# Optimization experiments

Hardware: AMD Instinct MI355X
Metric: run time of the kernel (lower is better)

## Reference

```python
import jax, jax.numpy as jnp
import numpy as np


def setup_inputs() -> dict:
    key = jax.random.key(0)
    k1, k2 = jax.random.split(key)
    B, F, L = 2048, 1, 512       # batch, n_features, seq_len
    N = 100000                   # fitted training windows
    x_enc = jax.random.normal(k1, (B, F, L), dtype=jnp.float32)
    X_fit = jax.random.normal(k2, (N, F * L), dtype=jnp.float32)
    return {"x_enc": x_enc, "X_fit": X_fit, "n_neighbors": 5}


def reference(x_enc, X_fit, n_neighbors):
    # x_enc: [B, F, L]; X_fit: [N, F*L]
    B, F, L = x_enc.shape
    q = x_enc.reshape(B, -1)                       # [B, D]
    # Squared Euclidean distances: ||q||^2 + ||x||^2 - 2 q.x^T  -> [B, N]
    q_sq = jnp.sum(q * q, axis=-1, keepdims=True)           # [B, 1]
    x_sq = jnp.sum(X_fit * X_fit, axis=-1)[None, :]         # [1, N]
    d2 = q_sq + x_sq - 2.0 * jnp.einsum("bd,nd->bn", q, X_fit)
    # k nearest = k smallest distances
    _, idx = jax.lax.top_k(-d2, n_neighbors)                # idx: [B, k]
    neigh = X_fit[idx]                                      # [B, k, D]
    y_hat = jnp.mean(neigh, axis=1).reshape(B, F, L)        # neighbor mean
    return y_hat
```

## Files before the change

kernel.cpp:

```cpp
#include <hip/hip_runtime.h>
#include <float.h>

#define D 512
#define BM 128
#define BN 256
#define BK 32
#define NCH 64
#define MPC 8
#define TR 16

typedef __attribute__((ext_vector_type(8))) short short8;
typedef __attribute__((ext_vector_type(4))) float f32x4;
typedef const __attribute__((address_space(1))) void gv_t;
typedef __attribute__((address_space(3))) void lv_t;

__device__ __forceinline__ void gl2lds16(const void* g, void* l) {
    __builtin_amdgcn_global_load_lds((gv_t*)g, (lv_t*)l, 16, 0, 0);
}

__device__ __forceinline__ unsigned short f2bf(float f) {
    unsigned u = __float_as_uint(f);
    return (unsigned short)((u + 0x7FFF + ((u >> 16) & 1)) >> 16);
}

template <int K>
__device__ __forceinline__ void insertK(float* bs, int* bi, float v, int id) {
    if (v < bs[K - 1]) {
        bs[K - 1] = v; bi[K - 1] = id;
#pragma unroll
        for (int r = K - 1; r >= 1; --r) {
            if (bs[r] < bs[r - 1]) {
                float tf = bs[r]; bs[r] = bs[r - 1]; bs[r - 1] = tf;
                int ti = bi[r]; bi[r] = bi[r - 1]; bi[r - 1] = ti;
            }
        }
    }
}

__global__ void convert_x(const float* __restrict__ X, unsigned short* __restrict__ Xbf,
                          float* __restrict__ xsq, int N, int padN) {
    int row = blockIdx.x * 4 + (threadIdx.x >> 6);
    int lane = threadIdx.x & 63;
    if (row >= padN) return;
    unsigned short ob[8];
    float s = 0.0f;
    if (row < N) {
        const float* p = X + (size_t)row * D + lane * 8;
        float4 a = *(const float4*)p;
        float4 b = *(const float4*)(p + 4);
        s = a.x * a.x + a.y * a.y + a.z * a.z + a.w * a.w
          + b.x * b.x + b.y * b.y + b.z * b.z + b.w * b.w;
        ob[0] = f2bf(a.x); ob[1] = f2bf(a.y); ob[2] = f2bf(a.z); ob[3] = f2bf(a.w);
        ob[4] = f2bf(b.x); ob[5] = f2bf(b.y); ob[6] = f2bf(b.z); ob[7] = f2bf(b.w);
    } else {
#pragma unroll
        for (int i = 0; i < 8; ++i) ob[i] = 0;
    }
    *(uint4*)(Xbf + (size_t)row * D + lane * 8) = *(uint4*)ob;
#pragma unroll
    for (int off = 32; off > 0; off >>= 1) s += __shfl_down(s, off, 64);
    if (lane == 0) xsq[row] = (row < N) ? s : 1e30f;
}

__global__ void convert_q(const float* __restrict__ Q, unsigned short* __restrict__ Qbf) {
    int row = blockIdx.x * 4 + (threadIdx.x >> 6);
    int lane = threadIdx.x & 63;
    const float* p = Q + (size_t)row * D + lane * 8;
    float4 a = *(const float4*)p;
    float4 b = *(const float4*)(p + 4);
    unsigned short ob[8];
    ob[0] = f2bf(-2.0f * a.x); ob[1] = f2bf(-2.0f * a.y);
    ob[2] = f2bf(-2.0f * a.z); ob[3] = f2bf(-2.0f * a.w);
    ob[4] = f2bf(-2.0f * b.x); ob[5] = f2bf(-2.0f * b.y);
    ob[6] = f2bf(-2.0f * b.z); ob[7] = f2bf(-2.0f * b.w);
    *(uint4*)(Qbf + (size_t)row * D + lane * 8) = *(uint4*)ob;
}

struct KBuf { unsigned short A[BM * BK]; unsigned short B[BN * BK]; };

#define STAGE(bp_, nn0, kk0)                                                          \
    do {                                                                              \
        const size_t kof_ = (size_t)(kk0) + sseg;                                     \
        gl2lds16(Qbf + (size_t)(qrow0 + srow) * D + kof_, (bp_)->A + wave * 512);     \
        gl2lds16(Qbf + (size_t)(qrow0 + 64 + srow) * D + kof_,                        \
                 (bp_)->A + 2048 + wave * 512);                                       \
        gl2lds16(Xbf + (size_t)((nn0) + srow) * D + kof_, (bp_)->B + wave * 512);     \
        gl2lds16(Xbf + (size_t)((nn0) + 64 + srow) * D + kof_,                        \
                 (bp_)->B + 2048 + wave * 512);                                       \
        gl2lds16(Xbf + (size_t)((nn0) + 128 + srow) * D + kof_,                       \
                 (bp_)->B + 4096 + wave * 512);                                       \
        gl2lds16(Xbf + (size_t)((nn0) + 192 + srow) * D + kof_,                       \
                 (bp_)->B + 6144 + wave * 512);                                       \
    } while (0)

#define COMPUTE(cbp_)                                                                 \
    do {                                                                              \
        const KBuf* cb_ = (cbp_);                                                     \
        short8 af_[4], bfr_[8];                                                       \
        _Pragma("unroll") for (int ti = 0; ti < 4; ++ti)                              \
            af_[ti] = *(const short8*)&cb_->A[(wm * 64 + ti * 16 + l15) * BK + kxor]; \
        _Pragma("unroll") for (int tj = 0; tj < 8; ++tj)                              \
            bfr_[tj] = *(const short8*)&cb_->B[(wn * 128 + tj * 16 + l15) * BK + kxor];\
        _Pragma("unroll") for (int ti = 0; ti < 4; ++ti)                              \
            _Pragma("unroll") for (int tj = 0; tj < 8; ++tj)                          \
                acc[ti][tj] = __builtin_amdgcn_mfma_f32_16x16x32_bf16(                \
                    af_[ti], bfr_[tj], acc[ti][tj], 0, 0, 0);                         \
    } while (0)

__global__ __launch_bounds__(256, 2) void score_mfma(
    const unsigned short* __restrict__ Qbf,
    const unsigned short* __restrict__ Xbf,
    const float* __restrict__ xsq,
    float* __restrict__ candS, int* __restrict__ candI,
    int ntiles)
{
    __shared__ struct {
        KBuf st[2];
        union {
            float scw[4][16 * 64];
            struct { float ms[4][64][MPC]; int mi[4][64][MPC]; } mg;
        } u2;
    } s;

    const int tid = threadIdx.x;
    const int wave = tid >> 6;
    const int lane = tid & 63;
    const int quad = lane >> 4;
    const int l15 = lane & 15;
    const int wm = wave & 1;
    const int wn = wave >> 1;

    const int bid = blockIdx.x;
    const int t = bid >> 3;
    const int chunk = (bid & 7) + 8 * (t >> 4);
    const int qt = t & 15;
    const int qrow0 = qt * BM;

    const int srow = tid >> 2;
    const int sseg = (((tid & 3) ^ ((tid >> 3) & 3)) * 8);
    const int kxor = ((quad ^ ((l15 >> 1) & 3)) * 8);
    const int xsw = (l15 & 7) << 2;

    float ts[MPC]; int ti8[MPC];
#pragma unroll
    for (int r = 0; r < MPC; ++r) { ts[r] = FLT_MAX; ti8[r] = -1; }

    float* scw = s.u2.scw[wave];

    int cur = 0;
    STAGE(&s.st[0], chunk * BN, 0);

    for (int tile = chunk; tile < ntiles; tile += NCH) {
        const int n0 = tile * BN;
        const bool last = (tile + NCH) >= ntiles;

        f32x4 acc[4][8];
#pragma unroll
        for (int tj = 0; tj < 8; ++tj) {
            float v = xsq[n0 + wn * 128 + tj * 16 + l15];
            f32x4 vv = {v, v, v, v};
#pragma unroll
            for (int ti = 0; ti < 4; ++ti) acc[ti][tj] = vv;
        }

        for (int ks = 0; ks < 15; ++ks) {
            __syncthreads();
            STAGE(&s.st[cur ^ 1], n0, (ks + 1) * BK);
            COMPUTE(&s.st[cur]);
            cur ^= 1;
        }
        __syncthreads();
        if (!last) STAGE(&s.st[cur ^ 1], n0 + NCH * BN, 0);
        COMPUTE(&s.st[cur]);
        cur ^= 1;

#pragma unroll
        for (int tj = 0; tj < 8; ++tj) {
#pragma unroll
            for (int ti = 0; ti < 4; ++ti)
                *(f32x4*)&scw[l15 * 64 + ((ti * 16 + quad * 4) ^ xsw)] = acc[ti][tj];
            const int cb0 = n0 + wn * 128 + tj * 16;
#pragma unroll 4
            for (int n = 0; n < 16; ++n) {
                float v = scw[n * 64 + (lane ^ ((n & 7) << 2))];
                insertK<MPC>(ts, ti8, v, cb0 + n);
            }
        }
    }

    __syncthreads();
#pragma unroll
    for (int r = 0; r < MPC; ++r) { s.u2.mg.ms[wave][lane][r] = ts[r]; s.u2.mg.mi[wave][lane][r] = ti8[r]; }
    __syncthreads();
    if (wn == 0) {
#pragma unroll
        for (int r = 0; r < MPC; ++r)
            insertK<MPC>(ts, ti8, s.u2.mg.ms[wave + 2][lane][r], s.u2.mg.mi[wave + 2][lane][r]);
        size_t base = ((size_t)(qrow0 + wm * 64 + lane) * NCH + chunk) * MPC;
#pragma unroll
        for (int r = 0; r < MPC; ++r) { candS[base + r] = ts[r]; candI[base + r] = ti8[r]; }
    }
}

__global__ void rescore_kernel(const float* __restrict__ Q, const float* __restrict__ X,
                               const float* __restrict__ xsq,
                               const float* __restrict__ candS, const int* __restrict__ candI,
                               float* __restrict__ out) {
    const int b = blockIdx.x;
    const int tid = threadIdx.x;
    const int wave = tid >> 6;
    const int lane = tid & 63;
    __shared__ int exI[TR];
    __shared__ float exS[TR];
    __shared__ int top5[5];

    if (wave == 0) {
        const float* cs = candS + (size_t)b * NCH * MPC;
        const int* ci = candI + (size_t)b * NCH * MPC;
        int h = 0;
        float cur = cs[lane * MPC];
        for (int r = 0; r < TR; ++r) {
            float v = cur; int wl = lane;
#pragma unroll
            for (int off = 1; off < 64; off <<= 1) {
                float ov = __shfl_xor(v, off, 64);
                int owl = __shfl_xor(wl, off, 64);
                if (ov < v || (ov == v && owl < wl)) { v = ov; wl = owl; }
            }
            if (lane == wl) {
                exI[r] = ci[lane * MPC + h];
                ++h;
                cur = (h < MPC) ? cs[lane * MPC + h] : FLT_MAX;
            }
        }
    }
    __syncthreads();

    const float* qr = Q + (size_t)b * D;
#pragma unroll
    for (int cc = 0; cc < 4; ++cc) {
        int c = wave * 4 + cc;
        int idx = exI[c];
        const float* xr = X + (size_t)idx * D;
        float4 qa = *(const float4*)(qr + lane * 8);
        float4 qb = *(const float4*)(qr + lane * 8 + 4);
        float4 xa = *(const float4*)(xr + lane * 8);
        float4 xb = *(const float4*)(xr + lane * 8 + 4);
        float p = qa.x * xa.x + qa.y * xa.y + qa.z * xa.z + qa.w * xa.w
                + qb.x * xb.x + qb.y * xb.y + qb.z * xb.z + qb.w * xb.w;
#pragma unroll
        for (int off = 32; off > 0; off >>= 1) p += __shfl_down(p, off, 64);
        if (lane == 0) exS[c] = xsq[idx] - 2.0f * p;
    }
    __syncthreads();

    if (tid == 0) {
        float fs[5]; int fi[5];
#pragma unroll
        for (int r = 0; r < 5; ++r) { fs[r] = FLT_MAX; fi[r] = -1; }
        for (int i = 0; i < TR; ++i) insertK<5>(fs, fi, exS[i], exI[i]);
#pragma unroll
        for (int r = 0; r < 5; ++r) top5[r] = fi[r];
    }
    __syncthreads();

#pragma unroll
    for (int dd = 0; dd < 2; ++dd) {
        int d = tid + dd * 256;
        float sacc = 0.0f;
#pragma unroll
        for (int r = 0; r < 5; ++r) sacc += X[(size_t)top5[r] * D + d];
        out[(size_t)b * D + d] = sacc / 5.0f;
    }
}

extern "C" void kernel_launch(void* const* d_in, const int* in_sizes, int n_in,
                              void* d_out, int out_size, void* d_ws, size_t ws_size,
                              hipStream_t stream) {
    const float* x_enc = (const float*)d_in[0];
    const float* X_fit = (const float*)d_in[1];
    float* out = (float*)d_out;
    const int B = in_sizes[0] / D;
    const int N = in_sizes[1] / D;
    const int padN = ((N + BN - 1) / BN) * BN;
    const int ntiles = padN / BN;
    const int qtiles = B / BM;

    char* w = (char*)d_ws;
    unsigned short* Xbf = (unsigned short*)w;            w += (size_t)padN * D * 2;
    unsigned short* Qbf = (unsigned short*)w;            w += (size_t)B * D * 2;
    float* xsq = (float*)w;                              w += (size_t)padN * 4;
    float* candS = (float*)w;                            w += (size_t)B * NCH * MPC * 4;
    int* candI = (int*)w;

    hipLaunchKernelGGL(convert_x, dim3(padN / 4), dim3(256), 0, stream, X_fit, Xbf, xsq, N, padN);
    hipLaunchKernelGGL(convert_q, dim3(B / 4), dim3(256), 0, stream, x_enc, Qbf);
    hipLaunchKernelGGL(score_mfma, dim3(qtiles * NCH), dim3(256), 0, stream,
                       Qbf, Xbf, xsq, candS, candI, ntiles);
    hipLaunchKernelGGL(rescore_kernel, dim3(B), dim3(256), 0, stream,
                       x_enc, X_fit, xsq, candS, candI, out);
}
```

Measured before the change: 938.3 us.

## Alias score scratch into staging buffers and relax barriers for higher occupancy

Removes the separate LDS region for the score scratch and merge arrays by aliasing them onto the idle staging buffer, which shrinks shared memory per block. Launch bounds rise to three blocks per CU. The K loop swaps __syncthreads for raw s_barrier plus an explicit vmcnt wait, so the next stage's global loads can stay in flight. The xsq bias is now added after the MFMA loop instead of seeding the accumulators. The higher occupancy target may force register spills given the large accumulator array, and the manual vmcnt counts must match the number of loads STAGE issues.

```diff
diff --git a/kernel.cpp b/kernel.cpp
--- a/kernel.cpp
+++ b/kernel.cpp
@@ -107,20 +107,14 @@
                     af_[ti], bfr_[tj], acc[ti][tj], 0, 0, 0);                         \
     } while (0)
 
-__global__ __launch_bounds__(256, 2) void score_mfma(
+__global__ __launch_bounds__(256, 3) void score_mfma(
     const unsigned short* __restrict__ Qbf,
     const unsigned short* __restrict__ Xbf,
     const float* __restrict__ xsq,
     float* __restrict__ candS, int* __restrict__ candI,
     int ntiles)
 {
-    __shared__ struct {
-        KBuf st[2];
-        union {
-            float scw[4][16 * 64];
-            struct { float ms[4][64][MPC]; int mi[4][64][MPC]; } mg;
-        } u2;
-    } s;
+    __shared__ KBuf st[2];
 
     const int tid = threadIdx.x;
     const int wave = tid >> 6;
@@ -145,10 +139,8 @@
 #pragma unroll
     for (int r = 0; r < MPC; ++r) { ts[r] = FLT_MAX; ti8[r] = -1; }
 
-    float* scw = s.u2.scw[wave];
-
     int cur = 0;
-    STAGE(&s.st[0], chunk * BN, 0);
+    STAGE(&st[0], chunk * BN, 0);
 
     for (int tile = chunk; tile < ntiles; tile += NCH) {
         const int n0 = tile * BN;
@@ -156,29 +148,42 @@
 
         f32x4 acc[4][8];
 #pragma unroll
+        for (int ti = 0; ti < 4; ++ti)
+#pragma unroll
+            for (int tj = 0; tj < 8; ++tj) acc[ti][tj] = (f32x4){0.f, 0.f, 0.f, 0.f};
+
+#pragma unroll 1
+        for (int ks = 0; ks < 15; ++ks) {
+            __builtin_amdgcn_s_barrier();
+            STAGE(&st[cur ^ 1], n0, (ks + 1) * BK);
+            asm volatile("s_waitcnt vmcnt(6)" ::: "memory");
+            __builtin_amdgcn_s_barrier();
+            COMPUTE(&st[cur]);
+            cur ^= 1;
+        }
+        __builtin_amdgcn_s_barrier();
+        if (!last) {
+            STAGE(&st[cur ^ 1], n0 + NCH * BN, 0);
+            asm volatile("s_waitcnt vmcnt(6)" ::: "memory");
+        } else {
+            asm volatile("s_waitcnt vmcnt(0)" ::: "memory");
+        }
+        __builtin_amdgcn_s_barrier();
+        COMPUTE(&st[cur]);
+        cur ^= 1;
+
+        __syncthreads();
+
+        float* scw = (float*)&st[cur ^ 1] + wave * 1024;
+#pragma unroll
         for (int tj = 0; tj < 8; ++tj) {
-            float v = xsq[n0 + wn * 128 + tj * 16 + l15];
-            f32x4 vv = {v, v, v, v};
-#pragma unroll
-            for (int ti = 0; ti < 4; ++ti) acc[ti][tj] = vv;
-        }
-
-        for (int ks = 0; ks < 15; ++ks) {
-            __syncthreads();
-            STAGE(&s.st[cur ^ 1], n0, (ks + 1) * BK);
-            COMPUTE(&s.st[cur]);
-            cur ^= 1;
-        }
-        __syncthreads();
-        if (!last) STAGE(&s.st[cur ^ 1], n0 + NCH * BN, 0);
-        COMPUTE(&s.st[cur]);
-        cur ^= 1;
-
-#pragma unroll
-        for (int tj = 0; tj < 8; ++tj) {
-#pragma unroll
-            for (int ti = 0; ti < 4; ++ti)
-                *(f32x4*)&scw[l15 * 64 + ((ti * 16 + quad * 4) ^ xsw)] = acc[ti][tj];
+            const float xvt = xsq[n0 + wn * 128 + tj * 16 + l15];
+#pragma unroll
+            for (int ti = 0; ti < 4; ++ti) {
+                f32x4 a = acc[ti][tj];
+                a.x += xvt; a.y += xvt; a.z += xvt; a.w += xvt;
+                *(f32x4*)&scw[l15 * 64 + ((ti * 16 + quad * 4) ^ xsw)] = a;
+            }
             const int cb0 = n0 + wn * 128 + tj * 16;
 #pragma unroll 4
             for (int n = 0; n < 16; ++n) {
@@ -189,13 +194,15 @@
     }
 
     __syncthreads();
-#pragma unroll
-    for (int r = 0; r < MPC; ++r) { s.u2.mg.ms[wave][lane][r] = ts[r]; s.u2.mg.mi[wave][lane][r] = ti8[r]; }
+    float (*ms)[MPC] = (float (*)[MPC])st;
+    int (*mi)[MPC] = (int (*)[MPC])((char*)st + 8192);
+#pragma unroll
+    for (int r = 0; r < MPC; ++r) { ms[tid][r] = ts[r]; mi[tid][r] = ti8[r]; }
     __syncthreads();
     if (wn == 0) {
 #pragma unroll
         for (int r = 0; r < MPC; ++r)
-            insertK<MPC>(ts, ti8, s.u2.mg.ms[wave + 2][lane][r], s.u2.mg.mi[wave + 2][lane][r]);
+            insertK<MPC>(ts, ti8, ms[tid + 128][r], mi[tid + 128][r]);
         size_t base = ((size_t)(qrow0 + wm * 64 + lane) * NCH + chunk) * MPC;
 #pragma unroll
         for (int r = 0; r < MPC; ++r) { candS[base + r] = ts[r]; candI[base + r] = ti8[r]; }
```

After: 1.698 ms. 81.0% more time.
